# Optimization experiments

Measured on AMD Instinct MI355X. Metric: run time of the kernel, lower is better.

## Reference

```python
import jax, jax.numpy as jnp
import numpy as np
import math

D = 256
NS = 64
KNB = 8
VOCAB = 32000
B, S = 4, 1024
NEG = -10000.0


def _normalize(x, eps=1e-12):
    n = jnp.linalg.norm(x, axis=-1, keepdims=True)
    return x / jnp.maximum(n, eps)


def _sparsemax(z):
    # sparsemax along last axis (descending sort + cumsum threshold)
    z_sorted = -jnp.sort(-z, axis=-1)
    cumsum = jnp.cumsum(z_sorted, axis=-1)
    k = jnp.arange(1, z.shape[-1] + 1, dtype=z.dtype)
    z_check = (1.0 + k * z_sorted > cumsum).astype(z.dtype)
    k_z = z_check.sum(axis=-1, keepdims=True)
    tau = (jnp.take_along_axis(cumsum, (k_z - 1).astype(jnp.int32), axis=-1) - 1.0) / k_z
    return jnp.clip(z - tau, 0.0)


def setup_inputs() -> dict:
    key = jax.random.key(0)
    ks = jax.random.split(key, 16)
    inp = {
        'messages': jax.random.normal(ks[0], (B, S, D), jnp.float32),
        'hidden': jax.random.normal(ks[1], (B, S, D), jnp.float32),
        'x_ids': jax.random.randint(ks[2], (B, S), 0, VOCAB),
        'scn': jax.random.normal(ks[3], (B, S, NS), jnp.float32),
        'mask': jax.random.bernoulli(ks[4], 0.3, (S, S)),
        'static_nb': jax.random.randint(ks[5], (VOCAB, KNB), 0, VOCAB),
        'geo_velocity': jax.random.normal(ks[6], (B, S, NS), jnp.float32),
        'ctx_conf': jax.random.uniform(ks[7], (B, S, 1), jnp.float32),
        'current_entropy': jax.random.uniform(ks[8], (B, S), jnp.float32) * math.log(VOCAB),
        # parameters (torch Linear weight layout: [out, in])
        'W_vel': jax.random.normal(ks[9], (D, NS), jnp.float32) / np.sqrt(NS),
        'W_e1': jax.random.normal(ks[10], (8, 1), jnp.float32),
        'b_e1': jax.random.normal(ks[11], (8,), jnp.float32) * 0.1,
        'W_e2': jax.random.normal(ks[12], (1, 8), jnp.float32) / np.sqrt(8),
        'b_e2': jax.random.normal(ks[13], (1,), jnp.float32) * 0.1,
        'W_probe': jax.random.normal(ks[14], (D, D), jnp.float32) / np.sqrt(D),
        'W_gate': jnp.zeros((1, D), jnp.float32),
        'b_gate': jnp.full((1,), -4.0, jnp.float32),
    }
    return inp


def reference(messages, hidden, x_ids, scn, mask, static_nb, geo_velocity,
              ctx_conf, current_entropy, W_vel, W_e1, b_e1, W_e2, b_e2,
              W_probe, W_gate, b_gate):
    Bd, Sd, Dh = messages.shape
    f32 = messages.dtype
    blocked = (mask | jnp.eye(Sd, dtype=bool))[None]  # [1,S,S] mask + diagonal

    # ---- geo branch ----
    endpoint = _normalize(scn + 0.4 * geo_velocity)
    endpoint_sim = jnp.einsum('bsn,btn->bst', endpoint, scn)
    endpoint_sim = jnp.where(blocked, NEG, endpoint_sim)
    H_norm = jax.lax.stop_gradient(current_entropy)[..., None] / (math.log(VOCAB) + 1e-8)
    vel_h = geo_velocity @ W_vel.T
    h_aimed = _normalize(hidden + 0.3 * vel_h)
    h_msg_sim = jnp.einsum('bsd,btd->bst', h_aimed, messages)
    combined_geo = (endpoint_sim * H_norm + 0.5 * h_msg_sim) * 5.0
    combined_geo = jnp.where(blocked, NEG, combined_geo)
    ew_geo = _sparsemax(combined_geo)
    geo_agg = jnp.einsum('bst,btd->bsd', ew_geo, messages)

    # ---- static neighbor-vocab branch ----
    nb_vocab = static_nb[x_ids]  # [B,S,Knb]
    match = (x_ids[:, None, None, :] == nb_vocab[..., None]).astype(f32)  # [B,S,Knb,S]
    causal = jnp.tril(jnp.ones((Sd, Sd), f32))
    match = match * causal[None, :, None, :]
    coverage = jnp.minimum(match.sum(-1), 1.0).mean(-1, keepdims=True)  # [B,S,1]
    nb_msgs_s = jnp.einsum('bskp,bpd->bskd', match, messages)
    nb_scn_s = jnp.einsum('bskp,bpn->bskn', match, scn)
    sim_s = (nb_scn_s * scn[:, :, None, :]).sum(-1)  # [B,S,Knb]
    h_e = jax.nn.gelu(sim_s[..., None] @ W_e1.T + b_e1, approximate=False)
    edge_out = (h_e @ W_e2.T + b_e2)[..., 0]  # [B,S,Knb]
    ew_s = jax.nn.softmax(edge_out, axis=-1)
    static_agg = (nb_msgs_s * ew_s[..., None]).sum(2)

    # ---- local mode branch ----
    my_mode = jnp.argmax(scn, axis=-1)
    same_mode = (my_mode[:, :, None] == my_mode[:, None, :]).astype(f32)
    same_mode = jnp.where(blocked, 0.0, same_mode)
    scn_sim = jnp.einsum('bsn,btn->bst', scn, scn) * same_mode
    has_nb = same_mode.sum(-1, keepdims=True) > 0
    pos = jnp.arange(Sd, dtype=f32)
    pos_sim = -jnp.abs(pos[:, None] - pos[None, :])[None]
    pos_sim = jnp.where(blocked, NEG, pos_sim)
    routing_sim = jnp.where(has_nb, scn_sim, pos_sim * 0.01)
    routing_sim = jnp.where(blocked, NEG, routing_sim)
    ew_l = _sparsemax(routing_sim * 5.0)
    local_agg = jnp.einsum('bst,btd->bsd', ew_l, messages)

    # ---- gated fusion ----
    static_final = coverage * static_agg + (1.0 - coverage) * local_agg
    raw_gate = jax.nn.sigmoid(hidden @ W_gate.T + b_gate)
    geo_weight = raw_gate * ctx_conf
    agg = geo_weight * geo_agg + (1.0 - geo_weight) * static_final
    probe = _normalize(hidden @ W_probe.T)
    agg_n = _normalize(agg)
    rel = jax.nn.sigmoid((agg_n * probe).sum(-1, keepdims=True))
    return agg * rel
```

## Files before the change

### kernel.cpp

```cpp
#include <hip/hip_runtime.h>
#include <math.h>

#define D_ 256
#define NS_ 64
#define KNB_ 8
#define SEQ_ 1024
#define B_ 4
#define MAXQ_ 1024
#define NEG_ (-10000.0f)
#define BLKNEG_ (-50000.0f)

#define MSGP_B 262144
#define SCNP_B 65536
#define ASTEPS 12

typedef short bf16x8 __attribute__((ext_vector_type(8)));
typedef float f32x4 __attribute__((ext_vector_type(4)));

__device__ __forceinline__ float waveSum(float v) {
#pragma unroll
    for (int off = 32; off; off >>= 1) v += __shfl_xor(v, off, 64);
    return v;
}

__device__ __forceinline__ void waveSum2(float& a, float& b) {
#pragma unroll
    for (int off = 32; off; off >>= 1) {
        a += __shfl_xor(a, off, 64);
        b += __shfl_xor(b, off, 64);
    }
}

__device__ __forceinline__ float blockSum(float v, float* scr) {
    const int tid = threadIdx.x;
    const int wid = tid >> 6, lane = tid & 63;
    v = waveSum(v);
    __syncthreads();
    if (lane == 0) scr[wid] = v;
    __syncthreads();
    return scr[0] + scr[1] + scr[2] + scr[3];
}

__device__ __forceinline__ void blockSum4(float v[4], float (*scr4)[4]) {
    const int tid = threadIdx.x;
    const int wid = tid >> 6, lane = tid & 63;
#pragma unroll
    for (int off = 32; off; off >>= 1) {
#pragma unroll
        for (int q = 0; q < 4; ++q) v[q] += __shfl_xor(v[q], off, 64);
    }
    __syncthreads();
    if (lane == 0) {
#pragma unroll
        for (int q = 0; q < 4; ++q) scr4[wid][q] = v[q];
    }
    __syncthreads();
#pragma unroll
    for (int q = 0; q < 4; ++q)
        v[q] = scr4[0][q] + scr4[1][q] + scr4[2][q] + scr4[3][q];
}

__device__ __forceinline__ float sparsemaxTauWave(const float* zr) {
    float mx = zr[0];
#pragma unroll
    for (int i = 1; i < 16; ++i) mx = fmaxf(mx, zr[i]);
#pragma unroll
    for (int off = 32; off; off >>= 1) mx = fmaxf(mx, __shfl_xor(mx, off, 64));
    float tau = mx - 1.0f;
    for (int it = 0; it < 32; ++it) {
        float ssum = 0.f, cnt = 0.f;
#pragma unroll
        for (int i = 0; i < 16; ++i) {
            if (zr[i] > tau) { ssum += zr[i]; cnt += 1.f; }
        }
        waveSum2(ssum, cnt);
        if (cnt < 0.5f) break;
        const float nt = (ssum - 1.0f) / cnt;
        if (nt == tau) break;
        tau = nt;
    }
    return tau;
}

__device__ __forceinline__ void cvtSplit(float a, short& h, short& l) {
    const unsigned ab = __float_as_uint(a);
    h = (short)(ab >> 16);
    const float hf = __uint_as_float(ab & 0xFFFF0000u);
    l = (short)(__float_as_uint(a - hf) >> 16);
}

__device__ __forceinline__ size_t aIdx(int sg, int st, int kq, int m16, int j) {
    return ((((size_t)sg * ASTEPS + st) << 6) + (kq << 4) + m16) * 8 + j;
}

__global__ __launch_bounds__(256) void setup_kernel(
    const float* __restrict__ messages, const float* __restrict__ scn,
    const float* __restrict__ hidden, const float* __restrict__ gvel,
    const float* __restrict__ ctx, const float* __restrict__ ent,
    const float* __restrict__ W_probe, const float* __restrict__ W_vel,
    const float* __restrict__ W_gate, const float* __restrict__ b_gate,
    short* __restrict__ msgH, short* __restrict__ msgL,
    short* __restrict__ scnH, short* __restrict__ scnL,
    const unsigned int* __restrict__ maskW, int* __restrict__ flag,
    int* __restrict__ qMeta,
    short* __restrict__ wsAh, short* __restrict__ wsAl,
    float* __restrict__ wsProbe,
    int* __restrict__ wsMode, float* __restrict__ wsGw)
{
    const int bid = blockIdx.x;
    const int tid = threadIdx.x;

    if (bid < 256) {
        const int b = bid >> 6, T = bid & 63;
        const float* src = messages + (size_t)b * SEQ_ * D_;
        short* dh = msgH + (size_t)b * MSGP_B;
        short* dl = msgL + (size_t)b * MSGP_B;
#pragma unroll
        for (int it = 0; it < 2; ++it) {
            const int g = (it << 8) + tid;
            const int st = g >> 6, kq = (g >> 4) & 3, m16 = g & 15;
            const int t = (T << 4) + m16;
            const int k0 = (st << 5) + (kq << 3);
            const float4 v0 = *(const float4*)(src + (size_t)t * D_ + k0);
            const float4 v1 = *(const float4*)(src + (size_t)t * D_ + k0 + 4);
            short h[8], l[8];
            cvtSplit(v0.x, h[0], l[0]); cvtSplit(v0.y, h[1], l[1]);
            cvtSplit(v0.z, h[2], l[2]); cvtSplit(v0.w, h[3], l[3]);
            cvtSplit(v1.x, h[4], l[4]); cvtSplit(v1.y, h[5], l[5]);
            cvtSplit(v1.z, h[6], l[6]); cvtSplit(v1.w, h[7], l[7]);
            const size_t o = (((size_t)T * 8 + st) << 9) + (size_t)((kq << 4) + m16) * 8;
            *(short4*)(dh + o) = make_short4(h[0], h[1], h[2], h[3]);
            *(short4*)(dh + o + 4) = make_short4(h[4], h[5], h[6], h[7]);
            *(short4*)(dl + o) = make_short4(l[0], l[1], l[2], l[3]);
            *(short4*)(dl + o + 4) = make_short4(l[4], l[5], l[6], l[7]);
// ... 87 lines not shown
        wsAh[aIdx(sg, stE, kqE, m16, jE)] = hh;
        wsAl[aIdx(sg, stE, kqE, m16, jE)] = ll;
        cvtSplit(5.0f * sv, hh, ll);
        wsAh[aIdx(sg, 2 + stE, kqE, m16, jE)] = hh;
        wsAl[aIdx(sg, 2 + stE, kqE, m16, jE)] = ll;
        float v = sv; int idx = lane;
#pragma unroll
        for (int off = 1; off < 64; off <<= 1) {
            const float ov = __shfl_xor(v, off, 64);
            const int   oi = __shfl_xor(idx, off, 64);
            if (ov > v || (ov == v && oi < idx)) { v = ov; idx = oi; }
        }
        float gd = 0.f;
#pragma unroll
        for (int j = 0; j < 4; ++j) {
            const int d = lane + (j << 6);
            gd = fmaf(h0[(size_t)r * D_ + d], W_gate[d], gd);
        }
        gd = waveSum(gd);
        if (lane == 0) {
            wsMode[row] = idx;
            const float raw = 1.f / (1.f + expf(-(gd + b_gate[0])));
            wsGw[row] = raw * ctx[row];
        }
    }

    const int stH = 4 + (tid >> 5), kqH = (tid & 31) >> 3, jH = tid & 7;
#pragma unroll
    for (int g = 0; g < 2; ++g) {
        float ha4[4], va[4], vp[4];
#pragma unroll
        for (int q = 0; q < 4; ++q) {
            const int r = (g << 2) + q;
            ha4[q] = h0[(size_t)r * D_ + tid] + 0.3f * vh[r];
            va[q] = ha4[q] * ha4[q];
            vp[q] = pr[(g << 2) + q] * pr[(g << 2) + q];
        }
        blockSum4(va, scr4);
        blockSum4(vp, scr4);
#pragma unroll
        for (int q = 0; q < 4; ++q) {
            const int r = (g << 2) + q;
            const int row = rowBase + r;
            const int sg = row >> 4, m16 = row & 15;
            short hh, ll;
            cvtSplit((ha4[q] / fmaxf(sqrtf(va[q]), 1e-12f)) * 2.5f, hh, ll);
            wsAh[aIdx(sg, stH, kqH, m16, jH)] = hh;
            wsAl[aIdx(sg, stH, kqH, m16, jH)] = ll;
            wsProbe[(size_t)row * D_ + tid] = pr[r] / fmaxf(sqrtf(vp[q]), 1e-12f);
        }
    }
}

__global__ __launch_bounds__(512) void sims_kernel(
    const short* __restrict__ msgH, const short* __restrict__ msgL,
    const short* __restrict__ scnH, const short* __restrict__ scnL,
    const short* __restrict__ wsAh, const short* __restrict__ wsAl,
    const int* __restrict__ wsMode,
    const void* __restrict__ maskP,
    const int* __restrict__ maskFlag,
    float* __restrict__ zgO,
    float* __restrict__ zlO)
{
    const int bid = blockIdx.x;
    const int half = bid & 1;
    const int sg = (bid >> 1) & 63;
    const int b = bid >> 7;
    const int sBase = sg << 4;
    const int rowBase = (b << 10) + sBase;
    const int tid = threadIdx.x;
    const int w = tid >> 6, l = tid & 63;
    const int m16 = l & 15, kq = l >> 4;
    const int l8 = l << 3;

    const int sgA = (b << 6) + sg;
    const short* AhB = wsAh + (size_t)sgA * (ASTEPS * 512) + l8;
    const short* AlB = wsAl + (size_t)sgA * (ASTEPS * 512) + l8;

    f32x4 accG[4], accL8[4];
#pragma unroll
    for (int ct = 0; ct < 4; ++ct) {
        accG[ct] = (f32x4){0.f, 0.f, 0.f, 0.f};
        accL8[ct] = (f32x4){0.f, 0.f, 0.f, 0.f};
    }

#pragma unroll
    for (int st = 0; st < 2; ++st) {
        const bf16x8 aeh = *(const bf16x8*)(AhB + (st << 9));
        const bf16x8 ael = *(const bf16x8*)(AlB + (st << 9));
        const bf16x8 ash = *(const bf16x8*)(AhB + ((2 + st) << 9));
        const bf16x8 asl = *(const bf16x8*)(AlB + ((2 + st) << 9));
#pragma unroll
        for (int ct = 0; ct < 4; ++ct) {
            const int mtile = (half << 5) + (w << 2) + ct;
            const size_t bo = (size_t)b * SCNP_B + (((size_t)mtile * 2 + st) << 9) + l8;
            const bf16x8 bh = *(const bf16x8*)(scnH + bo);
            const bf16x8 bl = *(const bf16x8*)(scnL + bo);
            accG[ct] = __builtin_amdgcn_mfma_f32_16x16x32_bf16(aeh, bh, accG[ct], 0, 0, 0);
            accG[ct] = __builtin_amdgcn_mfma_f32_16x16x32_bf16(aeh, bl, accG[ct], 0, 0, 0);
            accG[ct] = __builtin_amdgcn_mfma_f32_16x16x32_bf16(ael, bh, accG[ct], 0, 0, 0);
            accL8[ct] = __builtin_amdgcn_mfma_f32_16x16x32_bf16(ash, bh, accL8[ct], 0, 0, 0);
            accL8[ct] = __builtin_amdgcn_mfma_f32_16x16x32_bf16(ash, bl, accL8[ct], 0, 0, 0);
            accL8[ct] = __builtin_amdgcn_mfma_f32_16x16x32_bf16(asl, bh, accL8[ct], 0, 0, 0);
        }
    }
#pragma unroll
    for (int st = 0; st < 8; ++st) {
        const bf16x8 ah = *(const bf16x8*)(AhB + ((4 + st) << 9));
        const bf16x8 al = *(const bf16x8*)(AlB + ((4 + st) << 9));
#pragma unroll
        for (int ct = 0; ct < 4; ++ct) {
            const int mtile = (half << 5) + (w << 2) + ct;
            const size_t bo = (size_t)b * MSGP_B + (((size_t)mtile * 8 + st) << 9) + l8;
            const bf16x8 bh = *(const bf16x8*)(msgH + bo);
            const bf16x8 bl = *(const bf16x8*)(msgL + bo);
            accG[ct] = __builtin_amdgcn_mfma_f32_16x16x32_bf16(ah, bh, accG[ct], 0, 0, 0);
            accG[ct] = __builtin_amdgcn_mfma_f32_16x16x32_bf16(ah, bl, accG[ct], 0, 0, 0);
            accG[ct] = __builtin_amdgcn_mfma_f32_16x16x32_bf16(al, bh, accG[ct], 0, 0, 0);
        }
    }

    const int tBase = (half << 9) + (w << 6);
    const int mf = *maskFlag;
    const int4 mS4 = *(const int4*)(wsMode + rowBase + (kq << 2));
    const int mSq[4] = {mS4.x, mS4.y, mS4.z, mS4.w};
#pragma unroll
    for (int ct = 0; ct < 4; ++ct) {
        const int t = tBase + (ct << 4) + m16;
        const int mdt = wsMode[(b << 10) + t];
#pragma unroll
        for (int q = 0; q < 4; ++q) {
            const int r = (kq << 2) + q;
            const int s_r = sBase + r;
            const size_t mb = (size_t)s_r * SEQ_ + t;
            int blk;
            if (mf == 1)      blk = ((const unsigned char*)maskP)[mb] != 0;
            else if (mf == 2) blk = ((const float*)maskP)[mb] != 0.f;
            else              blk = ((const int*)maskP)[mb] != 0;
            if (s_r == t) blk = 1;
            zgO[(size_t)(rowBase + r) * SEQ_ + t] = blk ? NEG_ : accG[ct][q];
            const int sm = (!blk) && (mdt == mSq[q]);
            zlO[(size_t)(rowBase + r) * SEQ_ + t] =
                blk ? BLKNEG_ : (sm ? accL8[ct][q] : 0.0f);
        }
    }
}

__global__ __launch_bounds__(256) void route4_kernel(
    const float* __restrict__ messages,
    const float* __restrict__ scn,
    const int* __restrict__ x_ids,
    const int* __restrict__ static_nb,
    const float* __restrict__ W_e1,
    const float* __restrict__ b_e1,
    const float* __restrict__ W_e2,
    const float* __restrict__ b_e2,
    const float* __restrict__ wsProbe,
    const float* __restrict__ wsGw,
    const float* __restrict__ zgA,
    const float* __restrict__ zlA,
    float* __restrict__ wq,
    int* __restrict__ qRows,
    int* __restrict__ qMeta,
    float* __restrict__ out)
{
    __shared__ uint2 lst[4][256];
    __shared__ float ewLds[4][8];
    __shared__ int   mlist[4][64];

    const int jb = blockIdx.x;
    const int tid = threadIdx.x;
    const int wid = tid >> 6, lane = tid & 63;
    const int base = jb << 1;
    const int row = (wid == 0) ? base
                  : (wid == 1) ? base + 1
                  : (wid == 2) ? 4094 - base
                               : 4095 - base;
    const int b = row >> 10, s_r = row & 1023;
    const float* msgB = messages + (size_t)b * SEQ_ * D_;
    const float* scnB = scn + (size_t)b * SEQ_ * NS_;
    const unsigned long long ltmask = (1ull << lane) - 1ull;
    const int d4 = lane << 2;

    float zrG[16], zrL[16];
    {
        const float4* zgp = (const float4*)(zgA + (size_t)row * SEQ_ + (lane << 4));
        const float4* zlp = (const float4*)(zlA + (size_t)row * SEQ_ + (lane << 4));
#pragma unroll
        for (int q = 0; q < 4; ++q) {
            const float4 g4 = zgp[q];
            zrG[q * 4 + 0] = g4.x; zrG[q * 4 + 1] = g4.y;
            zrG[q * 4 + 2] = g4.z; zrG[q * 4 + 3] = g4.w;
            const float4 l4 = zlp[q];
            zrL[q * 4 + 0] = l4.x; zrL[q * 4 + 1] = l4.y;
            zrL[q * 4 + 2] = l4.z; zrL[q * 4 + 3] = l4.w;
        }
    }

    const int q = x_ids[row];
    int nb[KNB_];
#pragma unroll
    for (int k = 0; k < KNB_; ++k) nb[k] = static_nb[(size_t)q * KNB_ + k];
    const float ss_l = scnB[(size_t)s_r * NS_ + lane];
    float simk[KNB_] = {};
    unsigned matchedMask = 0;
    int mcW = 0;
    const int* xb = x_ids + (b << 10);
    for (int pb = 0; pb <= s_r; pb += 64) {
        const int p = pb + lane;
        const int id = (p <= s_r) ? xb[p] : -2147483647;
        unsigned kmask = 0;
#pragma unroll
        for (int k = 0; k < KNB_; ++k) kmask |= (id == nb[k]) ? (1u << k) : 0u;
        unsigned long long mb = __ballot(kmask != 0u);
        while (mb) {
            const int src = __ffsll(mb) - 1; mb &= mb - 1;
            const unsigned kms = (unsigned)__shfl((int)kmask, src, 64);
            const int pp = pb + src;
            float pv = scnB[(size_t)pp * NS_ + lane] * ss_l;
            pv = waveSum(pv);
            matchedMask |= kms;
#pragma unroll
            for (int k = 0; k < KNB_; ++k) {
                if ((kms >> k) & 1u) {
                    simk[k] += pv;
                    if (mcW < 64) { if (lane == 0) mlist[wid][mcW] = (pp << 3) | k; ++mcW; }
                }
            }
        }
    }
    const int kk = lane >> 3, jjn = lane & 7;
    float sv = simk[0];
#pragma unroll
    for (int k = 1; k < KNB_; ++k) sv = (kk == k) ? simk[k] : sv;
    const float xx = sv * W_e1[jjn] + b_e1[jjn];
    float eo = 0.5f * xx * (1.f + erff(xx * 0.70710678118654752f)) * W_e2[jjn];
    eo += __shfl_xor(eo, 1, 64); eo += __shfl_xor(eo, 2, 64); eo += __shfl_xor(eo, 4, 64);
    eo += b_e2[0];
    float m2 = eo;
    m2 = fmaxf(m2, __shfl_xor(m2, 8, 64));
    m2 = fmaxf(m2, __shfl_xor(m2, 16, 64));
    m2 = fmaxf(m2, __shfl_xor(m2, 32, 64));
    const float exv = expf(eo - m2);
    float smv = exv;
    smv += __shfl_xor(smv, 8, 64); smv += __shfl_xor(smv, 16, 64); smv += __shfl_xor(smv, 32, 64);
    if ((lane & 7) == 0) ewLds[wid][kk] = exv / smv;

    const float cov = (float)__popc(matchedMask) * 0.125f;
    const float gw = wsGw[row];
    const float coefG = gw;
    const float coefL = (1.f - gw) * (1.f - cov);
    const float coefS = (1.f - gw) * cov;

    int fl = 0;
#pragma unroll
    for (int j = 0; j < 16; ++j) fl |= (zrL[j] != 0.0f && zrL[j] > -40000.f);
    const int hasNb = __any(fl);
    if (!hasNb) {
#pragma unroll
        for (int j = 0; j < 16; ++j) {
            const int t = (lane << 4) + j;
            zrL[j] = (zrL[j] <= -40000.f) ? BLKNEG_ : -0.05f * fabsf((float)(s_r - t));
        }
    }

    const float tauG = sparsemaxTauWave(zrG);
    int supG = 0;
#pragma unroll
    for (int j = 0; j < 16; ++j) supG += __popcll(__ballot(zrG[j] > tauG));
    const float tauL = sparsemaxTauWave(zrL);
    int supL = 0;
#pragma unroll
    for (int j = 0; j < 16; ++j) supL += __popcll(__ballot(zrL[j] > tauL));
    const bool gDense = supG > 96;
    const bool lDense = supL > 96;

    int cnt = 0;
    if (!gDense) {
#pragma unroll
        for (int j = 0; j < 16; ++j) {
            const float wv = zrG[j] - tauG;
            const bool take = wv > 0.f;
            const unsigned long long m = __ballot(take);
            if (take) {
                const int pos = cnt + __popcll(m & ltmask);
                lst[wid][pos] = make_uint2((unsigned)((lane << 4) + j),
                                           __float_as_uint(coefG * wv));
            }
            cnt += __popcll(m);
        }
    }
    if (!lDense) {
#pragma unroll
        for (int j = 0; j < 16; ++j) {
            const float wv = zrL[j] - tauL;
            const bool take = wv > 0.f;
            const unsigned long long m = __ballot(take);
            if (take) {
                const int pos = cnt + __popcll(m & ltmask);
                lst[wid][pos] = make_uint2((unsigned)((lane << 4) + j),
                                           __float_as_uint(coefL * wv));
            }
            cnt += __popcll(m);
        }
    }
    const int nm = (mcW < 64) ? mcW : 64;
    for (int i = lane; i < nm; i += 64) {
        const int ee = mlist[wid][i];
        lst[wid][cnt + i] = make_uint2((unsigned)(ee >> 3),
                                       __float_as_uint(coefS * ewLds[wid][ee & 7]));
    }
    cnt += nm;

    float ox = 0.f, oy = 0.f, oz2 = 0.f, ow = 0.f;
    int i = 0;
    for (; i + 4 <= cnt; i += 4) {
        const uint2 e0 = lst[wid][i + 0];
        const uint2 e1 = lst[wid][i + 1];
        const uint2 e2 = lst[wid][i + 2];
        const uint2 e3 = lst[wid][i + 3];
        const float4 m0 = *(const float4*)(msgB + (size_t)e0.x * D_ + d4);
        const float4 m1 = *(const float4*)(msgB + (size_t)e1.x * D_ + d4);
        const float4 m2b = *(const float4*)(msgB + (size_t)e2.x * D_ + d4);
        const float4 m3 = *(const float4*)(msgB + (size_t)e3.x * D_ + d4);
        const float w0 = __uint_as_float(e0.y), w1 = __uint_as_float(e1.y);
        const float w2 = __uint_as_float(e2.y), w3 = __uint_as_float(e3.y);
        ox = fmaf(w0, m0.x, fmaf(w1, m1.x, fmaf(w2, m2b.x, fmaf(w3, m3.x, ox))));
        oy = fmaf(w0, m0.y, fmaf(w1, m1.y, fmaf(w2, m2b.y, fmaf(w3, m3.y, oy))));
        oz2 = fmaf(w0, m0.z, fmaf(w1, m1.z, fmaf(w2, m2b.z, fmaf(w3, m3.z, oz2))));
        ow = fmaf(w0, m0.w, fmaf(w1, m1.w, fmaf(w2, m2b.w, fmaf(w3, m3.w, ow))));
    }
    for (; i < cnt; ++i) {
        const uint2 e0 = lst[wid][i];
        const float w0 = __uint_as_float(e0.y);
        const float4 m0 = *(const float4*)(msgB + (size_t)e0.x * D_ + d4);
        ox = fmaf(w0, m0.x, ox); oy = fmaf(w0, m0.y, oy);
        oz2 = fmaf(w0, m0.z, oz2); ow = fmaf(w0, m0.w, ow);
    }

    int slot = -1;
    if (gDense || lDense) {
        int s0 = 0;
        if (lane == 0) s0 = atomicAdd(&qMeta[0], 1);
        slot = __shfl(s0, 0, 64);
    }
    if (slot >= 0 && slot < MAXQ_) {
#pragma unroll
        for (int qd = 0; qd < 4; ++qd) {
            float4 w4;
            float* wv4 = &w4.x;
#pragma unroll
            for (int u = 0; u < 4; ++u) {
                const int j = qd * 4 + u;
                float w = 0.f;
                if (gDense) w += coefG * fmaxf(zrG[j] - tauG, 0.f);
                if (lDense) w += coefL * fmaxf(zrL[j] - tauL, 0.f);
                wv4[u] = w;
            }
            *(float4*)(wq + (size_t)slot * SEQ_ + (lane << 4) + qd * 4) = w4;
        }
        if (lane == 0) qRows[slot] = row;
        *(float4*)(out + (size_t)row * D_ + d4) = make_float4(ox, oy, oz2, ow);
        return;
    }
    if (slot >= MAXQ_) {
#pragma unroll
        for (int j = 0; j < 16; ++j) {
            float wv = 0.f;
            if (gDense) wv += coefG * fmaxf(zrG[j] - tauG, 0.f);
            if (lDense) wv += coefL * fmaxf(zrL[j] - tauL, 0.f);
            unsigned long long m = __ballot(wv > 0.f);
            while (m) {
                const int s0 = __ffsll(m) - 1; m &= m - 1;
                const float w0 = __shfl(wv, s0, 64);
                const float4 m4 = *(const float4*)(msgB + (size_t)((s0 << 4) + j) * D_ + d4);
                ox = fmaf(w0, m4.x, ox); oy = fmaf(w0, m4.y, oy);
                oz2 = fmaf(w0, m4.z, oz2); ow = fmaf(w0, m4.w, ow);
            }
        }
    }

    float ssq = ox * ox + oy * oy + oz2 * oz2 + ow * ow;
    ssq = waveSum(ssq);
    const float nrm = fmaxf(sqrtf(ssq), 1e-12f);
    const float4 pr = *(const float4*)(wsProbe + (size_t)row * D_ + d4);
    float dp = (ox * pr.x + oy * pr.y + oz2 * pr.z + ow * pr.w) / nrm;
    dp = waveSum(dp);
    const float rel = 1.f / (1.f + expf(-dp));
    *(float4*)(out + (size_t)row * D_ + d4) =
        make_float4(ox * rel, oy * rel, oz2 * rel, ow * rel);
}

__global__ __launch_bounds__(256) void cleanup_kernel(
    const float* __restrict__ messages,
    const float* __restrict__ wsProbe,
    const float* __restrict__ wq,
    const int* __restrict__ qRows,
    int* __restrict__ qMeta,
    float* __restrict__ out)
{
    __shared__ float wsh[SEQ_];
    __shared__ float scr[4];
    __shared__ int idxSh;
    const int tid = threadIdx.x;
    const int nq = (qMeta[0] < MAXQ_) ? qMeta[0] : MAXQ_;
    for (;;) {
        __syncthreads();
        if (tid == 0) idxSh = atomicAdd(&qMeta[1], 1);
        __syncthreads();
        const int idx = idxSh;
        if (idx >= nq) break;
        const int row = qRows[idx];
        const int b = row >> 10;
        const float* msgB = messages + (size_t)b * SEQ_ * D_;
        for (int i = tid; i < SEQ_; i += 256)
            wsh[i] = wq[(size_t)idx * SEQ_ + i];
        __syncthreads();
        float acc = out[(size_t)row * D_ + tid];
        for (int t = 0; t < SEQ_; t += 4) {
            acc = fmaf(wsh[t + 0], msgB[(size_t)(t + 0) * D_ + tid],
                  fmaf(wsh[t + 1], msgB[(size_t)(t + 1) * D_ + tid],
                  fmaf(wsh[t + 2], msgB[(size_t)(t + 2) * D_ + tid],
                  fmaf(wsh[t + 3], msgB[(size_t)(t + 3) * D_ + tid], acc))));
        }
        const float ssq = blockSum(acc * acc, scr);
        const float nrm = fmaxf(sqrtf(ssq), 1e-12f);
        const float dp = blockSum((acc / nrm) * wsProbe[(size_t)row * D_ + tid], scr);
        const float rel = 1.f / (1.f + expf(-dp));
        out[(size_t)row * D_ + tid] = acc * rel;
    }
}

extern "C" void kernel_launch(void* const* d_in, const int* in_sizes, int n_in,
                              void* d_out, int out_size, void* d_ws, size_t ws_size,
                              hipStream_t stream) {
    const float* messages  = (const float*)d_in[0];
    const float* hidden    = (const float*)d_in[1];
    const int*   x_ids     = (const int*)d_in[2];
    const float* scn       = (const float*)d_in[3];
    const void*  mask      = d_in[4];
    const int*   static_nb = (const int*)d_in[5];
    const float* gvel      = (const float*)d_in[6];
    const float* ctx       = (const float*)d_in[7];
    const float* ent       = (const float*)d_in[8];
    const float* W_vel     = (const float*)d_in[9];
    const float* W_e1      = (const float*)d_in[10];
    const float* b_e1      = (const float*)d_in[11];
    const float* W_e2      = (const float*)d_in[12];
    const float* b_e2      = (const float*)d_in[13];
    const float* W_probe   = (const float*)d_in[14];
    const float* W_gate    = (const float*)d_in[15];
    const float* b_gate    = (const float*)d_in[16];
    float* out = (float*)d_out;
    (void)in_sizes; (void)n_in; (void)out_size; (void)ws_size;

    char* ws = (char*)d_ws;
    size_t o = 0;
    int* flag      = (int*)(ws + o);   o += 256;
    short* wsAh    = (short*)(ws + o); o += (size_t)B_ * SEQ_ * 384 * 2;
    short* wsAl    = (short*)(ws + o); o += (size_t)B_ * SEQ_ * 384 * 2;
    float* wsProbe = (float*)(ws + o); o += (size_t)B_ * SEQ_ * D_ * 4;
    int* wsMode    = (int*)(ws + o);   o += (size_t)B_ * SEQ_ * 4;
    float* wsGw    = (float*)(ws + o); o += (size_t)B_ * SEQ_ * 4;
    short* msgH    = (short*)(ws + o); o += (size_t)B_ * MSGP_B * 2;
    short* msgL    = (short*)(ws + o); o += (size_t)B_ * MSGP_B * 2;
    short* scnH    = (short*)(ws + o); o += (size_t)B_ * SCNP_B * 2;
    short* scnL    = (short*)(ws + o); o += (size_t)B_ * SCNP_B * 2;
    float* zgW     = (float*)(ws + o); o += (size_t)B_ * SEQ_ * SEQ_ * 4;
    float* zlW     = (float*)(ws + o); o += (size_t)B_ * SEQ_ * SEQ_ * 4;
    int* qMeta     = (int*)(ws + o);   o += 256;
    int* qRows     = (int*)(ws + o);   o += (size_t)MAXQ_ * 4;
    float* wq      = (float*)msgH;

    setup_kernel<<<dim3(833), dim3(256), 0, stream>>>(
        messages, scn, hidden, gvel, ctx, ent, W_probe, W_vel, W_gate, b_gate,
        msgH, msgL, scnH, scnL, (const unsigned int*)mask, flag, qMeta,
        wsAh, wsAl, wsProbe, wsMode, wsGw);
    sims_kernel<<<dim3(512), dim3(512), 0, stream>>>(
        msgH, msgL, scnH, scnL, wsAh, wsAl, wsMode, mask, flag, zgW, zlW);
    route4_kernel<<<dim3(B_ * SEQ_ / 4), dim3(256), 0, stream>>>(
        messages, scn, x_ids, static_nb, W_e1, b_e1, W_e2, b_e2,
        wsProbe, wsGw, zgW, zlW, wq, qRows, qMeta, out);
    cleanup_kernel<<<dim3(64), dim3(256), 0, stream>>>(
        messages, wsProbe, wq, qRows, qMeta, out);
}
```

Baseline: 111.2 us.

## Fuse similarity MFMA kernel with routing kernel via LDS-resident score tiles

Merges the similarity GEMM kernel and the per-row routing/sparsemax kernel into one kernel. Each block computes a 16-row by 1024-column score tile for both the geo and local branches, keeps it in LDS, and then routes those rows in place. This removes the two 16 MB global score matrices and one launch. In exchange, each block uses about 130 KB of LDS for 512 threads, the grid shrinks to 256 blocks, and each wave now handles two rows in sequence, which may cut occupancy and parallelism. The dense-row weight buffer also moves to its own workspace region instead of aliasing msgH.

Result: slower. 122.9 us (+10.6%).

```diff
diff --git a/kernel.cpp b/kernel.cpp
--- a/kernel.cpp
+++ b/kernel.cpp
@@ -9,6 +9,7 @@
 #define MAXQ_ 1024
 #define NEG_ (-10000.0f)
 #define BLKNEG_ (-50000.0f)
+#define ZP_ 1028
 
 #define MSGP_B 262144
 #define SCNP_B 65536
@@ -21,14 +22,6 @@
 #pragma unroll
     for (int off = 32; off; off >>= 1) v += __shfl_xor(v, off, 64);
     return v;
-}
-
-__device__ __forceinline__ void waveSum2(float& a, float& b) {
-#pragma unroll
-    for (int off = 32; off; off >>= 1) {
-        a += __shfl_xor(a, off, 64);
-        b += __shfl_xor(b, off, 64);
-    }
 }
 
 __device__ __forceinline__ float blockSum(float v, float* scr) {
@@ -58,28 +51,6 @@
 #pragma unroll
     for (int q = 0; q < 4; ++q)
         v[q] = scr4[0][q] + scr4[1][q] + scr4[2][q] + scr4[3][q];
-}
-
-__device__ __forceinline__ float sparsemaxTauWave(const float* zr) {
-    float mx = zr[0];
-#pragma unroll
-    for (int i = 1; i < 16; ++i) mx = fmaxf(mx, zr[i]);
-#pragma unroll
-    for (int off = 32; off; off >>= 1) mx = fmaxf(mx, __shfl_xor(mx, off, 64));
-    float tau = mx - 1.0f;
-    for (int it = 0; it < 32; ++it) {
-        float ssum = 0.f, cnt = 0.f;
-#pragma unroll
-        for (int i = 0; i < 16; ++i) {
-            if (zr[i] > tau) { ssum += zr[i]; cnt += 1.f; }
-        }
-        waveSum2(ssum, cnt);
-        if (cnt < 0.5f) break;
-        const float nt = (ssum - 1.0f) / cnt;
-        if (nt == tau) break;
-        tau = nt;
-    }
-    return tau;
 }
 
 __device__ __forceinline__ void cvtSplit(float a, short& h, short& l) {
@@ -273,101 +244,13 @@
     }
 }
 
-__global__ __launch_bounds__(512) void sims_kernel(
+__global__ __launch_bounds__(512) void fused_kernel(
     const short* __restrict__ msgH, const short* __restrict__ msgL,
     const short* __restrict__ scnH, const short* __restrict__ scnL,
     const short* __restrict__ wsAh, const short* __restrict__ wsAl,
     const int* __restrict__ wsMode,
     const void* __restrict__ maskP,
     const int* __restrict__ maskFlag,
-    float* __restrict__ zgO,
-    float* __restrict__ zlO)
-{
-    const int bid = blockIdx.x;
-    const int half = bid & 1;
-    const int sg = (bid >> 1) & 63;
-    const int b = bid >> 7;
-    const int sBase = sg << 4;
-    const int rowBase = (b << 10) + sBase;
-    const int tid = threadIdx.x;
-    const int w = tid >> 6, l = tid & 63;
-    const int m16 = l & 15, kq = l >> 4;
-    const int l8 = l << 3;
-
-    const int sgA = (b << 6) + sg;
-    const short* AhB = wsAh + (size_t)sgA * (ASTEPS * 512) + l8;
-    const short* AlB = wsAl + (size_t)sgA * (ASTEPS * 512) + l8;
-
-    f32x4 accG[4], accL8[4];
-#pragma unroll
-    for (int ct = 0; ct < 4; ++ct) {
-        accG[ct] = (f32x4){0.f, 0.f, 0.f, 0.f};
-        accL8[ct] = (f32x4){0.f, 0.f, 0.f, 0.f};
-    }
-
-#pragma unroll
-    for (int st = 0; st < 2; ++st) {
-        const bf16x8 aeh = *(const bf16x8*)(AhB + (st << 9));
-        const bf16x8 ael = *(const bf16x8*)(AlB + (st << 9));
-        const bf16x8 ash = *(const bf16x8*)(AhB + ((2 + st) << 9));
-        const bf16x8 asl = *(const bf16x8*)(AlB + ((2 + st) << 9));
-#pragma unroll
-        for (int ct = 0; ct < 4; ++ct) {
-            const int mtile = (half << 5) + (w << 2) + ct;
-            const size_t bo = (size_t)b * SCNP_B + (((size_t)mtile * 2 + st) << 9) + l8;
-            const bf16x8 bh = *(const bf16x8*)(scnH + bo);
-            const bf16x8 bl = *(const bf16x8*)(scnL + bo);
-            accG[ct] = __builtin_amdgcn_mfma_f32_16x16x32_bf16(aeh, bh, accG[ct], 0, 0, 0);
-            accG[ct] = __builtin_amdgcn_mfma_f32_16x16x32_bf16(aeh, bl, accG[ct], 0, 0, 0);
-            accG[ct] = __builtin_amdgcn_mfma_f32_16x16x32_bf16(ael, bh, accG[ct], 0, 0, 0);
-            accL8[ct] = __builtin_amdgcn_mfma_f32_16x16x32_bf16(ash, bh, accL8[ct], 0, 0, 0);
-            accL8[ct] = __builtin_amdgcn_mfma_f32_16x16x32_bf16(ash, bl, accL8[ct], 0, 0, 0);
-            accL8[ct] = __builtin_amdgcn_mfma_f32_16x16x32_bf16(asl, bh, accL8[ct], 0, 0, 0);
-        }
-    }
-#pragma unroll
-    for (int st = 0; st < 8; ++st) {
-        const bf16x8 ah = *(const bf16x8*)(AhB + ((4 + st) << 9));
-        const bf16x8 al = *(const bf16x8*)(AlB + ((4 + st) << 9));
-#pragma unroll
-        for (int ct = 0; ct < 4; ++ct) {
-            const int mtile = (half << 5) + (w << 2) + ct;
-            const size_t bo = (size_t)b * MSGP_B + (((size_t)mtile * 8 + st) << 9) + l8;
-            const bf16x8 bh = *(const bf16x8*)(msgH + bo);
-            const bf16x8 bl = *(const bf16x8*)(msgL + bo);
-            accG[ct] = __builtin_amdgcn_mfma_f32_16x16x32_bf16(ah, bh, accG[ct], 0, 0, 0);
-            accG[ct] = __builtin_amdgcn_mfma_f32_16x16x32_bf16(ah, bl, accG[ct], 0, 0, 0);
-            accG[ct] = __builtin_amdgcn_mfma_f32_16x16x32_bf16(al, bh, accG[ct], 0, 0, 0);
-        }
-    }
-
-    const int tBase = (half << 9) + (w << 6);
-    const int mf = *maskFlag;
-    const int4 mS4 = *(const int4*)(wsMode + rowBase + (kq << 2));
-    const int mSq[4] = {mS4.x, mS4.y, mS4.z, mS4.w};
-#pragma unroll
-    for (int ct = 0; ct < 4; ++ct) {
-        const int t = tBase + (ct << 4) + m16;
-        const int mdt = wsMode[(b << 10) + t];
-#pragma unroll
-        for (int q = 0; q < 4; ++q) {
-            const int r = (kq << 2) + q;
-            const int s_r = sBase + r;
-            const size_t mb = (size_t)s_r * SEQ_ + t;
-            int blk;
-            if (mf == 1)      blk = ((const unsigned char*)maskP)[mb] != 0;
-            else if (mf == 2) blk = ((const float*)maskP)[mb] != 0.f;
-            else              blk = ((const int*)maskP)[mb] != 0;
-            if (s_r == t) blk = 1;
-            zgO[(size_t)(rowBase + r) * SEQ_ + t] = blk ? NEG_ : accG[ct][q];
-            const int sm = (!blk) && (mdt == mSq[q]);
-            zlO[(size_t)(rowBase + r) * SEQ_ + t] =
-                blk ? BLKNEG_ : (sm ? accL8[ct][q] : 0.0f);
-        }
-    }
-}
-
-__global__ __launch_bounds__(256) void route4_kernel(
     const float* __restrict__ messages,
     const float* __restrict__ scn,
     const int* __restrict__ x_ids,
@@ -378,238 +261,327 @@
     const float* __restrict__ b_e2,
     const float* __restrict__ wsProbe,
     const float* __restrict__ wsGw,
-    const float* __restrict__ zgA,
-    const float* __restrict__ zlA,
     float* __restrict__ wq,
     int* __restrict__ qRows,
     int* __restrict__ qMeta,
     float* __restrict__ out)
 {
-    __shared__ uint2 lst[4][256];
-    __shared__ float ewLds[4][8];
-    __shared__ int   mlist[4][64];
-
-    const int jb = blockIdx.x;
+    __shared__ float zgS[16 * ZP_];
+    __shared__ float zlS[16 * ZP_];
+    __shared__ uint2 lst[8][256];
+    __shared__ float ewLds[8][8];
+    __shared__ int   mlist[8][64];
+
+    const int bid = blockIdx.x;
+    const int b = bid >> 6;
+    const int sg = bid & 63;
+    const int sBase = sg << 4;
+    const int rowBase = (b << 10) + sBase;
     const int tid = threadIdx.x;
-    const int wid = tid >> 6, lane = tid & 63;
-    const int base = jb << 1;
-    const int row = (wid == 0) ? base
-                  : (wid == 1) ? base + 1
-                  : (wid == 2) ? 4094 - base
-                               : 4095 - base;
-    const int b = row >> 10, s_r = row & 1023;
+    const int w = tid >> 6, l = tid & 63;
+    const int m16 = l & 15, kq = l >> 4;
+    const int l8 = l << 3;
+
+    {
+        const int sgA = (b << 6) + sg;
+        const short* AhB = wsAh + (size_t)sgA * (ASTEPS * 512) + l8;
+        const short* AlB = wsAl + (size_t)sgA * (ASTEPS * 512) + l8;
+
+        f32x4 accG[8], accL[8];
+#pragma unroll
+        for (int ct = 0; ct < 8; ++ct) {
+            accG[ct] = (f32x4){0.f, 0.f, 0.f, 0.f};
+            accL[ct] = (f32x4){0.f, 0.f, 0.f, 0.f};
+        }
+#pragma unroll
+        for (int st = 0; st < 2; ++st) {
+            const bf16x8 aeh = *(const bf16x8*)(AhB + (st << 9));
+            const bf16x8 ael = *(const bf16x8*)(AlB + (st << 9));
+            const bf16x8 ash = *(const bf16x8*)(AhB + ((2 + st) << 9));
+            const bf16x8 asl = *(const bf16x8*)(AlB + ((2 + st) << 9));
+#pragma unroll
+            for (int ct = 0; ct < 8; ++ct) {
+                const int mtile = (w << 3) + ct;
+                const size_t bo = (size_t)b * SCNP_B + (((size_t)mtile * 2 + st) << 9) + l8;
+                const bf16x8 bh = *(const bf16x8*)(scnH + bo);
+                const bf16x8 bl = *(const bf16x8*)(scnL + bo);
+                accG[ct] = __builtin_amdgcn_mfma_f32_16x16x32_bf16(aeh, bh, accG[ct], 0, 0, 0);
+                accG[ct] = __builtin_amdgcn_mfma_f32_16x16x32_bf16(aeh, bl, accG[ct], 0, 0, 0);
+                accG[ct] = __builtin_amdgcn_mfma_f32_16x16x32_bf16(ael, bh, accG[ct], 0, 0, 0);
+                accL[ct] = __builtin_amdgcn_mfma_f32_16x16x32_bf16(ash, bh, accL[ct], 0, 0, 0);
+                accL[ct] = __builtin_amdgcn_mfma_f32_16x16x32_bf16(ash, bl, accL[ct], 0, 0, 0);
+                accL[ct] = __builtin_amdgcn_mfma_f32_16x16x32_bf16(asl, bh, accL[ct], 0, 0, 0);
+            }
+        }
+#pragma unroll
+        for (int st = 0; st < 8; ++st) {
+            const bf16x8 ah = *(const bf16x8*)(AhB + ((4 + st) << 9));
+            const bf16x8 al = *(const bf16x8*)(AlB + ((4 + st) << 9));
+#pragma unroll
+            for (int ct = 0; ct < 8; ++ct) {
+                const int mtile = (w << 3) + ct;
+                const size_t bo = (size_t)b * MSGP_B + (((size_t)mtile * 8 + st) << 9) + l8;
+                const bf16x8 bh = *(const bf16x8*)(msgH + bo);
+                const bf16x8 bl = *(const bf16x8*)(msgL + bo);
+                accG[ct] = __builtin_amdgcn_mfma_f32_16x16x32_bf16(ah, bh, accG[ct], 0, 0, 0);
+                accG[ct] = __builtin_amdgcn_mfma_f32_16x16x32_bf16(ah, bl, accG[ct], 0, 0, 0);
+                accG[ct] = __builtin_amdgcn_mfma_f32_16x16x32_bf16(al, bh, accG[ct], 0, 0, 0);
+            }
+        }
+
+        const int mf = *maskFlag;
+        const int4 mS4 = *(const int4*)(wsMode + rowBase + (kq << 2));
+        const int mSq[4] = {mS4.x, mS4.y, mS4.z, mS4.w};
+#pragma unroll
+        for (int ct = 0; ct < 8; ++ct) {
+            const int t = (w << 7) + (ct << 4) + m16;
+            const int mdt = wsMode[(b << 10) + t];
+#pragma unroll
+            for (int q = 0; q < 4; ++q) {
+                const int r = (kq << 2) + q;
+                const int s_r = sBase + r;
+                const size_t mb = (size_t)s_r * SEQ_ + t;
+                int blk;
+                if (mf == 1)      blk = ((const unsigned char*)maskP)[mb] != 0;
+                else if (mf == 2) blk = ((const float*)maskP)[mb] != 0.f;
+                else              blk = ((const int*)maskP)[mb] != 0;
+                if (s_r == t) blk = 1;
+                zgS[r * ZP_ + t] = blk ? NEG_ : accG[ct][q];
+                const int sm = (!blk) && (mdt == mSq[q]);
+                zlS[r * ZP_ + t] = blk ? BLKNEG_ : (sm ? accL[ct][q] : 0.0f);
+            }
+        }
+    }
+    __syncthreads();
+
     const float* msgB = messages + (size_t)b * SEQ_ * D_;
     const float* scnB = scn + (size_t)b * SEQ_ * NS_;
-    const unsigned long long ltmask = (1ull << lane) - 1ull;
-    const int d4 = lane << 2;
-
-    float zrG[16], zrL[16];
-    {
-        const float4* zgp = (const float4*)(zgA + (size_t)row * SEQ_ + (lane << 4));
-        const float4* zlp = (const float4*)(zlA + (size_t)row * SEQ_ + (lane << 4));
-#pragma unroll
-        for (int q = 0; q < 4; ++q) {
-            const float4 g4 = zgp[q];
-            zrG[q * 4 + 0] = g4.x; zrG[q * 4 + 1] = g4.y;
-            zrG[q * 4 + 2] = g4.z; zrG[q * 4 + 3] = g4.w;
-            const float4 l4 = zlp[q];
-            zrL[q * 4 + 0] = l4.x; zrL[q * 4 + 1] = l4.y;
-            zrL[q * 4 + 2] = l4.z; zrL[q * 4 + 3] = l4.w;
-        }
-    }
-
-    const int q = x_ids[row];
-    int nb[KNB_];
-#pragma unroll
-    for (int k = 0; k < KNB_; ++k) nb[k] = static_nb[(size_t)q * KNB_ + k];
-    const float ss_l = scnB[(size_t)s_r * NS_ + lane];
-    float simk[KNB_] = {};
-    unsigned matchedMask = 0;
-    int mcW = 0;
-    const int* xb = x_ids + (b << 10);
-    for (int pb = 0; pb <= s_r; pb += 64) {
-        const int p = pb + lane;
-        const int id = (p <= s_r) ? xb[p] : -2147483647;
-        unsigned kmask = 0;
-#pragma unroll
-        for (int k = 0; k < KNB_; ++k) kmask |= (id == nb[k]) ? (1u << k) : 0u;
-        unsigned long long mb = __ballot(kmask != 0u);
-        while (mb) {
-            const int src = __ffsll(mb) - 1; mb &= mb - 1;
-            const unsigned kms = (unsigned)__shfl((int)kmask, src, 64);
-            const int pp = pb + src;
-            float pv = scnB[(size_t)pp * NS_ + lane] * ss_l;
-            pv = waveSum(pv);
-            matchedMask |= kms;
-#pragma unroll
-            for (int k = 0; k < KNB_; ++k) {
-                if ((kms >> k) & 1u) {
-                    simk[k] += pv;
-                    if (mcW < 64) { if (lane == 0) mlist[wid][mcW] = (pp << 3) | k; ++mcW; }
+    const unsigned long long ltmask = (1ull << l) - 1ull;
+    const int d4 = l << 2;
+
+    for (int rr = 0; rr < 2; ++rr) {
+        const int r = w + (rr << 3);
+        const int s_r = sBase + r;
+        const int row = rowBase + r;
+
+        float zrG[16], zrL[16];
+#pragma unroll
+        for (int j = 0; j < 16; ++j) {
+            zrG[j] = zgS[r * ZP_ + (j << 6) + l];
+            zrL[j] = zlS[r * ZP_ + (j << 6) + l];
+        }
+
+        const int q = x_ids[row];
+        int nb[KNB_];
+#pragma unroll
+        for (int k = 0; k < KNB_; ++k) nb[k] = static_nb[(size_t)q * KNB_ + k];
+        const float ss_l = scnB[(size_t)s_r * NS_ + l];
+        float simk[KNB_] = {};
+        unsigned matchedMask = 0;
+        int mcW = 0;
+        const int* xb = x_ids + (b << 10);
+        for (int pb = 0; pb <= s_r; pb += 64) {
+            const int p = pb + l;
+            const int id = (p <= s_r) ? xb[p] : -2147483647;
+            unsigned kmask = 0;
+#pragma unroll
+            for (int k = 0; k < KNB_; ++k) kmask |= (id == nb[k]) ? (1u << k) : 0u;
+            unsigned long long mb = __ballot(kmask != 0u);
+            while (mb) {
+                const int src = __ffsll(mb) - 1; mb &= mb - 1;
+                const unsigned kms = (unsigned)__shfl((int)kmask, src, 64);
+                const int pp = pb + src;
+                float pv = scnB[(size_t)pp * NS_ + l] * ss_l;
+                pv = waveSum(pv);
+                matchedMask |= kms;
+#pragma unroll
+                for (int k = 0; k < KNB_; ++k) {
+                    if ((kms >> k) & 1u) {
+                        simk[k] += pv;
+                        if (mcW < 64) { if (l == 0) mlist[w][mcW] = (pp << 3) | k; ++mcW; }
+                    }
                 }
             }
         }
-    }
-    const int kk = lane >> 3, jjn = lane & 7;
-    float sv = simk[0];
-#pragma unroll
-    for (int k = 1; k < KNB_; ++k) sv = (kk == k) ? simk[k] : sv;
-    const float xx = sv * W_e1[jjn] + b_e1[jjn];
-    float eo = 0.5f * xx * (1.f + erff(xx * 0.70710678118654752f)) * W_e2[jjn];
-    eo += __shfl_xor(eo, 1, 64); eo += __shfl_xor(eo, 2, 64); eo += __shfl_xor(eo, 4, 64);
-    eo += b_e2[0];
-    float m2 = eo;
-    m2 = fmaxf(m2, __shfl_xor(m2, 8, 64));
-    m2 = fmaxf(m2, __shfl_xor(m2, 16, 64));
-    m2 = fmaxf(m2, __shfl_xor(m2, 32, 64));
-    const float exv = expf(eo - m2);
-    float smv = exv;
-    smv += __shfl_xor(smv, 8, 64); smv += __shfl_xor(smv, 16, 64); smv += __shfl_xor(smv, 32, 64);
-    if ((lane & 7) == 0) ewLds[wid][kk] = exv / smv;
-
-    const float cov = (float)__popc(matchedMask) * 0.125f;
-    const float gw = wsGw[row];
-    const float coefG = gw;
-    const float coefL = (1.f - gw) * (1.f - cov);
-    const float coefS = (1.f - gw) * cov;
-
-    int fl = 0;
-#pragma unroll
-    for (int j = 0; j < 16; ++j) fl |= (zrL[j] != 0.0f && zrL[j] > -40000.f);
-    const int hasNb = __any(fl);
-    if (!hasNb) {
+        const int kk = l >> 3, jjn = l & 7;
+        float sv = simk[0];
+#pragma unroll
+        for (int k = 1; k < KNB_; ++k) sv = (kk == k) ? simk[k] : sv;
+        const float xx = sv * W_e1[jjn] + b_e1[jjn];
+        float eo = 0.5f * xx * (1.f + erff(xx * 0.70710678118654752f)) * W_e2[jjn];
+        eo += __shfl_xor(eo, 1, 64); eo += __shfl_xor(eo, 2, 64); eo += __shfl_xor(eo, 4, 64);
+        eo += b_e2[0];
+        float m2 = eo;
+        m2 = fmaxf(m2, __shfl_xor(m2, 8, 64));
+        m2 = fmaxf(m2, __shfl_xor(m2, 16, 64));
+        m2 = fmaxf(m2, __shfl_xor(m2, 32, 64));
+        const float exv = expf(eo - m2);
+        float smv = exv;
+        smv += __shfl_xor(smv, 8, 64); smv += __shfl_xor(smv, 16, 64); smv += __shfl_xor(smv, 32, 64);
+        if ((l & 7) == 0) ewLds[w][kk] = exv / smv;
+
+        const float cov = (float)__popc(matchedMask) * 0.125f;
+        const float gw = wsGw[row];
+        const float coefG = gw;
+        const float coefL = (1.f - gw) * (1.f - cov);
+        const float coefS = (1.f - gw) * cov;
+
+        int fl = 0;
+#pragma unroll
+        for (int j = 0; j < 16; ++j) fl |= (zrL[j] != 0.0f && zrL[j] > -40000.f);
+        const int hasNb = __any(fl);
+        if (!hasNb) {
+#pragma unroll
+            for (int j = 0; j < 16; ++j) {
+                const int t = (j << 6) + l;
+                zrL[j] = (zrL[j] <= -40000.f) ? BLKNEG_ : -0.05f * fabsf((float)(s_r - t));
+            }
+        }
+
+        float mxG = zrG[0], mxL = zrL[0];
+#pragma unroll
+        for (int j = 1; j < 16; ++j) { mxG = fmaxf(mxG, zrG[j]); mxL = fmaxf(mxL, zrL[j]); }
+#pragma unroll
+        for (int off = 32; off; off >>= 1) {
+            mxG = fmaxf(mxG, __shfl_xor(mxG, off, 64));
+            mxL = fmaxf(mxL, __shfl_xor(mxL, off, 64));
+        }
+        float tauG = mxG - 1.f, tauL = mxL - 1.f;
+        for (int it = 0; it < 32; ++it) {
+            float sG = 0.f, cG = 0.f, sL = 0.f, cL = 0.f;
+#pragma unroll
+            for (int j = 0; j < 16; ++j) {
+                if (zrG[j] > tauG) { sG += zrG[j]; cG += 1.f; }
+                if (zrL[j] > tauL) { sL += zrL[j]; cL += 1.f; }
+            }
+#pragma unroll
+            for (int off = 32; off; off >>= 1) {
+                sG += __shfl_xor(sG, off, 64); cG += __shfl_xor(cG, off, 64);
+                sL += __shfl_xor(sL, off, 64); cL += __shfl_xor(cL, off, 64);
+            }
+            const float nG = (sG - 1.f) / fmaxf(cG, 1.f);
+            const float nL = (sL - 1.f) / fmaxf(cL, 1.f);
+            if (nG == tauG && nL == tauL) break;
+            tauG = nG; tauL = nL;
+        }
+
+        int supG = 0, supL = 0;
 #pragma unroll
         for (int j = 0; j < 16; ++j) {
-            const int t = (lane << 4) + j;
-            zrL[j] = (zrL[j] <= -40000.f) ? BLKNEG_ : -0.05f * fabsf((float)(s_r - t));
-        }
-    }
-
-    const float tauG = sparsemaxTauWave(zrG);
-    int supG = 0;
-#pragma unroll
-    for (int j = 0; j < 16; ++j) supG += __popcll(__ballot(zrG[j] > tauG));
-    const float tauL = sparsemaxTauWave(zrL);
-    int supL = 0;
-#pragma unroll
-    for (int j = 0; j < 16; ++j) supL += __popcll(__ballot(zrL[j] > tauL));
-    const bool gDense = supG > 96;
-    const bool lDense = supL > 96;
-
-    int cnt = 0;
-    if (!gDense) {
-#pragma unroll
-        for (int j = 0; j < 16; ++j) {
-            const float wv = zrG[j] - tauG;
-            const bool take = wv > 0.f;
-            const unsigned long long m = __ballot(take);
-            if (take) {
-                const int pos = cnt + __popcll(m & ltmask);
-                lst[wid][pos] = make_uint2((unsigned)((lane << 4) + j),
-                                           __float_as_uint(coefG * wv));
-            }
-            cnt += __popcll(m);
-        }
-    }
-    if (!lDense) {
-#pragma unroll
-        for (int j = 0; j < 16; ++j) {
-            const float wv = zrL[j] - tauL;
-            const bool take = wv > 0.f;
-            const unsigned long long m = __ballot(take);
-            if (take) {
-                const int pos = cnt + __popcll(m & ltmask);
-                lst[wid][pos] = make_uint2((unsigned)((lane << 4) + j),
-                                           __float_as_uint(coefL * wv));
-            }
-            cnt += __popcll(m);
-        }
-    }
-    const int nm = (mcW < 64) ? mcW : 64;
-    for (int i = lane; i < nm; i += 64) {
-        const int ee = mlist[wid][i];
-        lst[wid][cnt + i] = make_uint2((unsigned)(ee >> 3),
-                                       __float_as_uint(coefS * ewLds[wid][ee & 7]));
-    }
-    cnt += nm;
-
-    float ox = 0.f, oy = 0.f, oz2 = 0.f, ow = 0.f;
-    int i = 0;
-    for (; i + 4 <= cnt; i += 4) {
-        const uint2 e0 = lst[wid][i + 0];
-        const uint2 e1 = lst[wid][i + 1];
-        const uint2 e2 = lst[wid][i + 2];
-        const uint2 e3 = lst[wid][i + 3];
-        const float4 m0 = *(const float4*)(msgB + (size_t)e0.x * D_ + d4);
-        const float4 m1 = *(const float4*)(msgB + (size_t)e1.x * D_ + d4);
-        const float4 m2b = *(const float4*)(msgB + (size_t)e2.x * D_ + d4);
-        const float4 m3 = *(const float4*)(msgB + (size_t)e3.x * D_ + d4);
-        const float w0 = __uint_as_float(e0.y), w1 = __uint_as_float(e1.y);
-        const float w2 = __uint_as_float(e2.y), w3 = __uint_as_float(e3.y);
-        ox = fmaf(w0, m0.x, fmaf(w1, m1.x, fmaf(w2, m2b.x, fmaf(w3, m3.x, ox))));
-        oy = fmaf(w0, m0.y, fmaf(w1, m1.y, fmaf(w2, m2b.y, fmaf(w3, m3.y, oy))));
-        oz2 = fmaf(w0, m0.z, fmaf(w1, m1.z, fmaf(w2, m2b.z, fmaf(w3, m3.z, oz2))));
-        ow = fmaf(w0, m0.w, fmaf(w1, m1.w, fmaf(w2, m2b.w, fmaf(w3, m3.w, ow))));
-    }
-    for (; i < cnt; ++i) {
-        const uint2 e0 = lst[wid][i];
-        const float w0 = __uint_as_float(e0.y);
-        const float4 m0 = *(const float4*)(msgB + (size_t)e0.x * D_ + d4);
-        ox = fmaf(w0, m0.x, ox); oy = fmaf(w0, m0.y, oy);
-        oz2 = fmaf(w0, m0.z, oz2); ow = fmaf(w0, m0.w, ow);
-    }
-
-    int slot = -1;
-    if (gDense || lDense) {
-        int s0 = 0;
-        if (lane == 0) s0 = atomicAdd(&qMeta[0], 1);
-        slot = __shfl(s0, 0, 64);
-    }
-    if (slot >= 0 && slot < MAXQ_) {
-#pragma unroll
-        for (int qd = 0; qd < 4; ++qd) {
-            float4 w4;
-            float* wv4 = &w4.x;
-#pragma unroll
-            for (int u = 0; u < 4; ++u) {
-                const int j = qd * 4 + u;
-                float w = 0.f;
-                if (gDense) w += coefG * fmaxf(zrG[j] - tauG, 0.f);
-                if (lDense) w += coefL * fmaxf(zrL[j] - tauL, 0.f);
-                wv4[u] = w;
-            }
-            *(float4*)(wq + (size_t)slot * SEQ_ + (lane << 4) + qd * 4) = w4;
-        }
-        if (lane == 0) qRows[slot] = row;
-        *(float4*)(out + (size_t)row * D_ + d4) = make_float4(ox, oy, oz2, ow);
-        return;
-    }
-    if (slot >= MAXQ_) {
-#pragma unroll
-        for (int j = 0; j < 16; ++j) {
-            float wv = 0.f;
-            if (gDense) wv += coefG * fmaxf(zrG[j] - tauG, 0.f);
-            if (lDense) wv += coefL * fmaxf(zrL[j] - tauL, 0.f);
-            unsigned long long m = __ballot(wv > 0.f);
-            while (m) {
-                const int s0 = __ffsll(m) - 1; m &= m - 1;
-                const float w0 = __shfl(wv, s0, 64);
-                const float4 m4 = *(const float4*)(msgB + (size_t)((s0 << 4) + j) * D_ + d4);
-                ox = fmaf(w0, m4.x, ox); oy = fmaf(w0, m4.y, oy);
-                oz2 = fmaf(w0, m4.z, oz2); ow = fmaf(w0, m4.w, ow);
-            }
-        }
-    }
-
-    float ssq = ox * ox + oy * oy + oz2 * oz2 + ow * ow;
-    ssq = waveSum(ssq);
-    const float nrm = fmaxf(sqrtf(ssq), 1e-12f);
-    const float4 pr = *(const float4*)(wsProbe + (size_t)row * D_ + d4);
-    float dp = (ox * pr.x + oy * pr.y + oz2 * pr.z + ow * pr.w) / nrm;
-    dp = waveSum(dp);
-    const float rel = 1.f / (1.f + expf(-dp));
-    *(float4*)(out + (size_t)row * D_ + d4) =
-        make_float4(ox * rel, oy * rel, oz2 * rel, ow * rel);
+            supG += __popcll(__ballot(zrG[j] > tauG));
+            supL += __popcll(__ballot(zrL[j] > tauL));
+        }
+        const bool gDense = supG > 96;
+        const bool lDense = supL > 96;
+
+        int cnt = 0;
+        if (!gDense) {
+#pragma unroll
+            for (int j = 0; j < 16; ++j) {
+                const float wv = zrG[j] - tauG;
+                const bool take = wv > 0.f;
+                const unsigned long long m = __ballot(take);
+                if (take) {
+                    const int pos = cnt + __popcll(m & ltmask);
+                    lst[w][pos] = make_uint2((unsigned)((j << 6) + l),
+                                             __float_as_uint(coefG * wv));
+                }
+                cnt += __popcll(m);
+            }
+        }
+        if (!lDense) {
+#pragma unroll
+            for (int j = 0; j < 16; ++j) {
+                const float wv = zrL[j] - tauL;
+                const bool take = wv > 0.f;
+                const unsigned long long m = __ballot(take);
+                if (take) {
+                    const int pos = cnt + __popcll(m & ltmask);
+                    lst[w][pos] = make_uint2((unsigned)((j << 6) + l),
+                                             __float_as_uint(coefL * wv));
+                }
+                cnt += __popcll(m);
+            }
+        }
+        const int nm = (mcW < 64) ? mcW : 64;
+        for (int i = l; i < nm; i += 64) {
+            const int ee = mlist[w][i];
+            lst[w][cnt + i] = make_uint2((unsigned)(ee >> 3),
+                                         __float_as_uint(coefS * ewLds[w][ee & 7]));
+        }
+        cnt += nm;
+
+        float ox = 0.f, oy = 0.f, oz2 = 0.f, ow = 0.f;
+        int i = 0;
+        for (; i + 4 <= cnt; i += 4) {
+            const uint2 e0 = lst[w][i + 0];
+            const uint2 e1 = lst[w][i + 1];
+            const uint2 e2 = lst[w][i + 2];
+            const uint2 e3 = lst[w][i + 3];
+            const float4 m0 = *(const float4*)(msgB + (size_t)e0.x * D_ + d4);
+            const float4 m1 = *(const float4*)(msgB + (size_t)e1.x * D_ + d4);
+            const float4 m2b = *(const float4*)(msgB + (size_t)e2.x * D_ + d4);
+            const float4 m3 = *(const float4*)(msgB + (size_t)e3.x * D_ + d4);
+            const float w0 = __uint_as_float(e0.y), w1 = __uint_as_float(e1.y);
+            const float w2 = __uint_as_float(e2.y), w3 = __uint_as_float(e3.y);
+            ox = fmaf(w0, m0.x, fmaf(w1, m1.x, fmaf(w2, m2b.x, fmaf(w3, m3.x, ox))));
+            oy = fmaf(w0, m0.y, fmaf(w1, m1.y, fmaf(w2, m2b.y, fmaf(w3, m3.y, oy))));
+            oz2 = fmaf(w0, m0.z, fmaf(w1, m1.z, fmaf(w2, m2b.z, fmaf(w3, m3.z, oz2))));
+            ow = fmaf(w0, m0.w, fmaf(w1, m1.w, fmaf(w2, m2b.w, fmaf(w3, m3.w, ow))));
+        }
+        for (; i < cnt; ++i) {
+            const uint2 e0 = lst[w][i];
+            const float w0 = __uint_as_float(e0.y);
+            const float4 m0 = *(const float4*)(msgB + (size_t)e0.x * D_ + d4);
+            ox = fmaf(w0, m0.x, ox); oy = fmaf(w0, m0.y, oy);
+            oz2 = fmaf(w0, m0.z, oz2); ow = fmaf(w0, m0.w, ow);
+        }
+
+        int slot = -1;
+        if (gDense || lDense) {
+            int s0 = 0;
+            if (l == 0) s0 = atomicAdd(&qMeta[0], 1);
+            slot = __shfl(s0, 0, 64);
+        }
+        if (slot >= 0 && slot < MAXQ_) {
+#pragma unroll
+            for (int j = 0; j < 16; ++j) {
+                float wv = 0.f;
+                if (gDense) wv += coefG * fmaxf(zrG[j] - tauG, 0.f);
+                if (lDense) wv += coefL * fmaxf(zrL[j] - tauL, 0.f);
+                wq[(size_t)slot * SEQ_ + (j << 6) + l] = wv;
+            }
+            if (l == 0) qRows[slot] = row;
+            *(float4*)(out + (size_t)row * D_ + d4) = make_float4(ox, oy, oz2, ow);
+            continue;
+        }
+        if (slot >= MAXQ_) {
+#pragma unroll
+            for (int j = 0; j < 16; ++j) {
+                float wv = 0.f;
+                if (gDense) wv += coefG * fmaxf(zrG[j] - tauG, 0.f);
+                if (lDense) wv += coefL * fmaxf(zrL[j] - tauL, 0.f);
+                unsigned long long m = __ballot(wv > 0.f);
+                while (m) {
+                    const int s0 = __ffsll(m) - 1; m &= m - 1;
+                    const float w0 = __shfl(wv, s0, 64);
+                    const float4 m4 = *(const float4*)(msgB + (size_t)((j << 6) + s0) * D_ + d4);
+                    ox = fmaf(w0, m4.x, ox); oy = fmaf(w0, m4.y, oy);
+                    oz2 = fmaf(w0, m4.z, oz2); ow = fmaf(w0, m4.w, ow);
+                }
+            }
+        }
+
+        float ssq = ox * ox + oy * oy + oz2 * oz2 + ow * ow;
+        ssq = waveSum(ssq);
+        const float nrm = fmaxf(sqrtf(ssq), 1e-12f);
+        const float4 pr = *(const float4*)(wsProbe + (size_t)row * D_ + d4);
+        float dp = (ox * pr.x + oy * pr.y + oz2 * pr.z + ow * pr.w) / nrm;
+        dp = waveSum(dp);
+        const float rel = 1.f / (1.f + expf(-dp));
+        *(float4*)(out + (size_t)row * D_ + d4) =
+            make_float4(ox * rel, oy * rel, oz2 * rel, ow * rel);
+    }
 }
 
 __global__ __launch_bounds__(256) void cleanup_kernel(
@@ -687,21 +659,18 @@
     short* msgL    = (short*)(ws + o); o += (size_t)B_ * MSGP_B * 2;
     short* scnH    = (short*)(ws + o); o += (size_t)B_ * SCNP_B * 2;
     short* scnL    = (short*)(ws + o); o += (size_t)B_ * SCNP_B * 2;
-    float* zgW     = (float*)(ws + o); o += (size_t)B_ * SEQ_ * SEQ_ * 4;
-    float* zlW     = (float*)(ws + o); o += (size_t)B_ * SEQ_ * SEQ_ * 4;
+    float* wq      = (float*)(ws + o); o += (size_t)MAXQ_ * SEQ_ * 4;
     int* qMeta     = (int*)(ws + o);   o += 256;
     int* qRows     = (int*)(ws + o);   o += (size_t)MAXQ_ * 4;
-    float* wq      = (float*)msgH;
 
     setup_kernel<<<dim3(833), dim3(256), 0, stream>>>(
         messages, scn, hidden, gvel, ctx, ent, W_probe, W_vel, W_gate, b_gate,
         msgH, msgL, scnH, scnL, (const unsigned int*)mask, flag, qMeta,
         wsAh, wsAl, wsProbe, wsMode, wsGw);
-    sims_kernel<<<dim3(512), dim3(512), 0, stream>>>(
-        msgH, msgL, scnH, scnL, wsAh, wsAl, wsMode, mask, flag, zgW, zlW);
-    route4_kernel<<<dim3(B_ * SEQ_ / 4), dim3(256), 0, stream>>>(
+    fused_kernel<<<dim3(256), dim3(512), 0, stream>>>(
+        msgH, msgL, scnH, scnL, wsAh, wsAl, wsMode, mask, flag,
         messages, scn, x_ids, static_nb, W_e1, b_e1, W_e2, b_e2,
-        wsProbe, wsGw, zgW, zlW, wq, qRows, qMeta, out);
+        wsProbe, wsGw, wq, qRows, qMeta, out);
     cleanup_kernel<<<dim3(64), dim3(256), 0, stream>>>(
         messages, wsProbe, wq, qRows, qMeta, out);
 }
```
